# Kernel optimization log

Hardware: AMD Instinct MI355X
Metric: run time of the kernel (lower is better)

The kernel has to match this reference:

```python
import math
import jax, jax.numpy as jnp
from jax import lax
import numpy as np

B, C, M, N = 8, 512, 64, 64
DN = ('NCHW', 'OIHW', 'NCHW')


def dct_mat(n):
    # Orthonormal DCT-II basis, matching the torch construction.
    i = jnp.arange(n, dtype=jnp.float32)
    A = jnp.cos(jnp.outer(i, i + 0.5) * (math.pi / n)) * np.float32(math.sqrt(2.0 / n))
    return A.at[0].divide(np.float32(math.sqrt(2.0)))


def setup_inputs() -> dict:
    key = jax.random.key(0)
    ks = jax.random.split(key, 7)
    s = 0.05
    x = jax.random.normal(ks[0], (B, C, M, N), dtype=jnp.float32)
    # 4 conv branches, each: 1x1 512->128, 3x3 dil=2 128->128, 1x1 128->128
    W1 = jax.random.normal(ks[1], (4, 128, 512, 1, 1), dtype=jnp.float32) * s
    b1 = jax.random.normal(ks[2], (4, 128), dtype=jnp.float32) * s
    W2 = jax.random.normal(ks[3], (4, 128, 128, 3, 3), dtype=jnp.float32) * s
    b2 = jax.random.normal(ks[4], (4, 128), dtype=jnp.float32) * s
    W3 = jax.random.normal(ks[5], (4, 128, 128, 1, 1), dtype=jnp.float32) * s
    b3 = jax.random.normal(ks[6], (4, 128), dtype=jnp.float32) * s
    return {"x": x, "W1": W1, "b1": b1, "W2": W2, "b2": b2, "W3": W3, "b3": b3}


def dct3d_topk(x):
    b, c, m, n = x.shape
    Ac, Ar, Ak = dct_mat(n), dct_mat(m), dct_mat(c)
    # separable 3D DCT: along N, then M, then C
    t = jnp.einsum('kn,bcmn->bcmk', Ac, x)
    t = jnp.einsum('km,bcmn->bckn', Ar, t)
    D = jnp.einsum('kc,bcmn->bkmn', Ak, t)
    total = b * c * m * n
    absD = jnp.abs(D)
    s = jnp.sort(absD.reshape(-1))  # ascending; kth-largest = s[total-k]
    recons = []
    for k in (total // 4, total // 16, total // 64, total // 256):
        thr = s[total - k]
        Dm = jnp.where(absD >= thr, D, jnp.float32(0))
        y = jnp.einsum('kc,bkmn->bcmn', Ak, Dm)   # inverse along C
        y = jnp.einsum('km,bckn->bcmn', Ar, y)    # inverse along M
        y = jnp.einsum('kn,bcmk->bcmn', Ac, y)    # inverse along N
        recons.append(y)
    return jnp.stack(recons)  # [4, B, C, M, N]


def conv_branch(h, w1, c1, w2, c2, w3, c3):
    h = lax.conv_general_dilated(h, w1, (1, 1), 'VALID', dimension_numbers=DN)
    h = jax.nn.relu(h + c1[None, :, None, None])
    h = lax.conv_general_dilated(h, w2, (1, 1), ((2, 2), (2, 2)), rhs_dilation=(2, 2), dimension_numbers=DN)
    h = jax.nn.relu(h + c2[None, :, None, None])
    h = lax.conv_general_dilated(h, w3, (1, 1), 'VALID', dimension_numbers=DN)
    return jax.nn.relu(h + c3[None, :, None, None])


def reference(x, W1, b1, W2, b2, W3, b3):
    d = dct3d_topk(x)
    outs = [conv_branch(d[i], W1[i], b1[i], W2[i], b2[i], W3[i], b3[i]) for i in range(4)]
    w = jax.nn.softmax(jnp.concatenate(outs, axis=1), axis=1)
    return x * w + x
```

## Files before the change

### kernel.cpp

```cpp
#include <hip/hip_runtime.h>
#include <math.h>

#define NB   8
#define NC   512
#define SP   4096
#define TOT  16777216L
static const double PI_D = 3.14159265358979323846;

typedef short s16x8 __attribute__((ext_vector_type(8)));
typedef float f32x4 __attribute__((ext_vector_type(4)));
typedef unsigned short u16;

#define OFF_T    0L
#define OFF_CAND 0L
#define OFF_CNT  8388608L
#define OFF_P2   8392704L
#define OFF_P3   9441280L
#define OFF_H2R  9965568L
#define OFF_H3R  9969664L
#define OFF_GF   9971712L
#define OFF_H1P  0L
#define OFF_X2   8388608L
#define OFF_THI  16777216L
#define OFF_H1   16777216L
#define OFF_D    25165824L
#define OFF_H2   25165824L
#define OFF_AKFH 41943040L
#define OFF_AKFL 42074112L
#define OFF_AKH  42205184L
#define OFF_AKL  42336256L
#define OFF_ACT  42467328L
#define OFF_GBF  42468352L
#define OFF_W2A  42599424L
#define OFF_W3B  42894336L
#define OFF_HIST 42927104L
#define OFF_SEL  42937344L
#define OFF_THR  42937360L
#define OFF_ACH  42937368L
#define OFF_ACL  42939416L

__device__ inline u16 bfr(float x) {
    unsigned u = __float_as_uint(x);
    unsigned r = u + 0x7fffu + ((u >> 16) & 1u);
    return (u16)(r >> 16);
}
__device__ inline float bff(u16 h) { return __uint_as_float(((unsigned)h) << 16); }

#define MFMA(a, b, c) __builtin_amdgcn_mfma_f32_16x16x32_bf16((a), (b), (c), 0, 0, 0)

__global__ void k_ctab(float* __restrict__ ctab) {
    int m = blockIdx.x * 256 + threadIdx.x;
    if (m < 2048) ctab[m] = (float)cos(PI_D * (double)m / 1024.0);
}

__global__ void k_build_mats(const float* __restrict__ ctab,
                             u16* __restrict__ Akh, u16* __restrict__ Akl,
                             u16* __restrict__ Akfh, u16* __restrict__ Akfl,
                             u16* __restrict__ AcT, u16* __restrict__ Ach, u16* __restrict__ Acl) {
    int idx = blockIdx.x * 256 + threadIdx.x;
    if (idx < 512 * 512) {
        int i = idx >> 9, j = idx & 511;
        float c = ctab[(i * (2 * j + 1)) & 2047];
        float f = c * (i == 0 ? 0.04419417382415922f : 0.0625f);
        u16 h = bfr(f);
        u16 l = bfr(f - bff(h));
        Akh[idx] = h;
        Akl[idx] = l;
        long fa = ((long)(i >> 4) * 16 + (j >> 5)) * 512 + ((j >> 3) & 3) * 128 + (i & 15) * 8 + (j & 7);
        Akfh[fa] = h;
        Akfl[fa] = l;
    }
    if (idx < 64 * 64) {
        int i = idx >> 6, j = idx & 63;
        float c = ctab[(8 * i * (2 * j + 1)) & 2047];
        float a = c * (i == 0 ? 0.125f : 0.17677669529663687f);
        u16 ah = bfr(a);
        Ach[idx] = ah;
        Acl[idx] = bfr(a - bff(ah));
        int n = idx >> 6, np = idx & 63;
        float w = ctab[(8 * np * (2 * n + 1)) & 2047];
        AcT[idx] = bfr(w * (np == 0 ? 0.125f : 0.17677669529663687f));
    }
}

__global__ void k_zero(unsigned* __restrict__ p, int n) {
    int i = blockIdx.x * 256 + threadIdx.x;
    if (i < n) p[i] = 0u;
}

__global__ __launch_bounds__(256, 2) void k_gmm(const float* __restrict__ W1,
                                                const u16* __restrict__ Akh, const u16* __restrict__ Akl,
                                                u16* __restrict__ G) {
    __shared__ __align__(16) short Wh[128 * 40];
    __shared__ __align__(16) short Wl[128 * 40];
    __shared__ __align__(16) short Qh[128 * 40];
    __shared__ __align__(16) short Ql[128 * 40];
    const int p0 = blockIdx.y * 128, kc0 = blockIdx.x * 128;
    const int tid = threadIdx.x;
    const int lane = tid & 63, wave = tid >> 6;
    const int fr = lane & 15, qd = lane >> 4;
    const int mq = (wave >> 1) * 64, nq = (wave & 1) * 64;
    f32x4 acc[4][4];
#pragma unroll
    for (int i = 0; i < 4; ++i)
#pragma unroll
        for (int j = 0; j < 4; ++j) acc[i][j] = (f32x4){0.f, 0.f, 0.f, 0.f};
    const float* Pg = W1 + (long)p0 * 512;
    const u16* Qgh = Akh + (long)kc0 * 512;
    const u16* Qgl = Akl + (long)kc0 * 512;
    const int r0 = tid >> 2, q40 = (tid & 3) * 8;
    float4 pa4[2], pb4[2];
    s16x8 qsh[2], qsl[2];
#pragma unroll
    for (int j = 0; j < 2; ++j) {
        int r = r0 + j * 64;
        const float* src = &Pg[(long)r * 512 + q40];
        pa4[j] = *(const float4*)src;
        pb4[j] = *(const float4*)(src + 4);
        qsh[j] = *(const s16x8*)&Qgh[(long)r * 512 + q40];
        qsl[j] = *(const s16x8*)&Qgl[(long)r * 512 + q40];
    }
    for (int ch = 0; ch < 16; ++ch) {
        __syncthreads();
#pragma unroll
        for (int j = 0; j < 2; ++j) {
            int r = r0 + j * 64;
            float f[8] = {pa4[j].x, pa4[j].y, pa4[j].z, pa4[j].w,
                          pb4[j].x, pb4[j].y, pb4[j].z, pb4[j].w};
            s16x8 vh, vl;
#pragma unroll
            for (int q = 0; q < 8; ++q) {
                u16 h = bfr(f[q]);
                vh[q] = (short)h;
                vl[q] = (short)bfr(f[q] - bff(h));
            }
            *(s16x8*)&Wh[r * 40 + q40] = vh;
            *(s16x8*)&Wl[r * 40 + q40] = vl;
            *(s16x8*)&Qh[r * 40 + q40] = qsh[j];
            *(s16x8*)&Ql[r * 40 + q40] = qsl[j];
        }
        __syncthreads();
        if (ch < 15) {
            const int kn = (ch + 1) * 32;
#pragma unroll
            for (int j = 0; j < 2; ++j) {
                int r = r0 + j * 64;
                const float* src = &Pg[(long)r * 512 + kn + q40];
                pa4[j] = *(const float4*)src;
                pb4[j] = *(const float4*)(src + 4);
                qsh[j] = *(const s16x8*)&Qgh[(long)r * 512 + kn + q40];
                qsl[j] = *(const s16x8*)&Qgl[(long)r * 512 + kn + q40];
            }
        }
// ... 129 lines not shown
    }
#pragma unroll
    for (int i = 0; i < 2; ++i)
#pragma unroll
        for (int j = 0; j < 2; ++j) {
            int k1 = nq + 16 * j + fr;
            int mb = mq + 16 * i + qd * 4;
            ushort4 ph, pl;
            float v0 = a1[i][j][0], v1 = a1[i][j][1], v2 = a1[i][j][2], v3 = a1[i][j][3];
            ph.x = bfr(v0); ph.y = bfr(v1); ph.z = bfr(v2); ph.w = bfr(v3);
            pl.x = bfr(v0 - bff(ph.x)); pl.y = bfr(v1 - bff(ph.y));
            pl.z = bfr(v2 - bff(ph.z)); pl.w = bfr(v3 - bff(ph.w));
            *(ushort4*)&Uh[k1 * 72 + mb] = ph;
            *(ushort4*)&Ul[k1 * 72 + mb] = pl;
        }
    __syncthreads();
    f32x4 a2[2][2];
#pragma unroll
    for (int i = 0; i < 2; ++i)
#pragma unroll
        for (int j = 0; j < 2; ++j) a2[i][j] = (f32x4){0.f, 0.f, 0.f, 0.f};
#pragma unroll
    for (int ks = 0; ks < 2; ++ks) {
        const int k0 = ks * 32 + qd * 8;
        s16x8 uh[2], ul[2];
#pragma unroll
        for (int i = 0; i < 2; ++i) {
            uh[i] = *(const s16x8*)&Uh[(mq + 16 * i + fr) * 72 + k0];
            ul[i] = *(const s16x8*)&Ul[(mq + 16 * i + fr) * 72 + k0];
        }
#pragma unroll
        for (int j = 0; j < 2; ++j) {
            s16x8 qh = *(const s16x8*)&Ah[(nq + 16 * j + fr) * 72 + k0];
            s16x8 ql = *(const s16x8*)&Al[(nq + 16 * j + fr) * 72 + k0];
#pragma unroll
            for (int i = 0; i < 2; ++i) {
                a2[i][j] = MFMA(uh[i], qh, a2[i][j]);
                a2[i][j] = MFMA(uh[i], ql, a2[i][j]);
                a2[i][j] = MFMA(ul[i], qh, a2[i][j]);
            }
        }
    }
#pragma unroll
    for (int i = 0; i < 2; ++i)
#pragma unroll
        for (int j = 0; j < 2; ++j) {
            int k2 = nq + 16 * j + fr;
            int nb = mq + 16 * i + qd * 4;
            ushort4 pk;
            pk.x = bfr(a2[i][j][0]); pk.y = bfr(a2[i][j][1]);
            pk.z = bfr(a2[i][j][2]); pk.w = bfr(a2[i][j][3]);
            *(ushort4*)&dst[k2 * 64 + nb] = pk;
        }
}

__global__ __launch_bounds__(256) void k_tsplit(const u16* __restrict__ t16,
                                                u16* __restrict__ thi) {
    __shared__ float Ls[64][65];
    const int b = blockIdx.z, cg = blockIdx.y, pg = blockIdx.x;
    const int tid = threadIdx.x;
    const u16* src = t16 + ((long)b * 512 + cg * 64) * 4096 + pg * 64;
#pragma unroll
    for (int j = 0; j < 2; ++j) {
        int idx = tid + j * 256;
        int c = idx >> 3, p8 = (idx & 7) * 8;
        s16x8 v = *(const s16x8*)&src[(long)c * 4096 + p8];
#pragma unroll
        for (int q = 0; q < 8; ++q) Ls[c][p8 + q] = bff((u16)v[q]);
    }
    __syncthreads();
#pragma unroll
    for (int j = 0; j < 2; ++j) {
        int idx = tid + j * 256;
        int p = idx >> 3, c8 = idx & 7;
        s16x8 vh;
#pragma unroll
        for (int q = 0; q < 8; ++q) vh[q] = (short)bfr(Ls[c8 * 8 + q][p]);
        long addr = ((long)b * 4096 + pg * 64 + p) * 512 + cg * 64 + c8 * 8;
        *(s16x8*)&thi[addr] = vh;
    }
}

__global__ __launch_bounds__(256, 4) void k_cgemm(const u16* __restrict__ thi,
                                                  const u16* __restrict__ Akfh, const u16* __restrict__ Akfl,
                                                  float* __restrict__ D, unsigned* __restrict__ g1) {
    __shared__ __align__(16) short Ph[128 * 40];
    __shared__ unsigned hh[2048];
    const int b = blockIdx.z;
    const int p0 = blockIdx.y * 128, kc0 = blockIdx.x * 128;
    const int tid = threadIdx.x;
    const int lane = tid & 63, wave = tid >> 6;
    const int fr = lane & 15, qd = lane >> 4;
    const int mq = (wave >> 1) * 64, nq = (wave & 1) * 64;
    for (int t = tid; t < 2048; t += 256) hh[t] = 0u;
    f32x4 acc[4][4];
#pragma unroll
    for (int i = 0; i < 4; ++i)
#pragma unroll
        for (int j = 0; j < 4; ++j) acc[i][j] = (f32x4){0.f, 0.f, 0.f, 0.f};
    const u16* Pgh = thi + ((long)b * 4096 + p0) * 512;
    const int r0 = tid >> 2, q40 = (tid & 3) * 8;
    s16x8 psh[2];
#pragma unroll
    for (int j = 0; j < 2; ++j)
        psh[j] = *(const s16x8*)&Pgh[(long)(r0 + j * 64) * 512 + q40];
    const long qb0 = ((long)(kc0 >> 4) + (nq >> 4)) * 16 * 512 + (long)lane * 8;
    for (int ch = 0; ch < 16; ++ch) {
        __syncthreads();
#pragma unroll
        for (int j = 0; j < 2; ++j)
            *(s16x8*)&Ph[(r0 + j * 64) * 40 + q40] = psh[j];
        __syncthreads();
        if (ch < 15) {
            const int kn = (ch + 1) * 32;
#pragma unroll
            for (int j = 0; j < 2; ++j)
                psh[j] = *(const s16x8*)&Pgh[(long)(r0 + j * 64) * 512 + kn + q40];
        }
        const long qbase = qb0 + (long)ch * 512;
        s16x8 qfh[4], qfl[4];
#pragma unroll
        for (int j = 0; j < 4; ++j) {
            qfh[j] = *(const s16x8*)&Akfh[qbase + (long)j * 8192];
            qfl[j] = *(const s16x8*)&Akfl[qbase + (long)j * 8192];
        }
#pragma unroll
        for (int i = 0; i < 4; ++i) {
            s16x8 ph = *(const s16x8*)&Ph[(mq + 16 * i + fr) * 40 + qd * 8];
#pragma unroll
            for (int j = 0; j < 4; ++j) {
                acc[i][j] = MFMA(ph, qfh[j], acc[i][j]);
                acc[i][j] = MFMA(ph, qfl[j], acc[i][j]);
            }
        }
    }
#pragma unroll
    for (int i = 0; i < 4; ++i)
#pragma unroll
        for (int j = 0; j < 4; ++j) {
            int rowb = mq + 16 * i + qd * 4;
            int col = kc0 + nq + 16 * j + fr;
#pragma unroll
            for (int r = 0; r < 4; ++r) {
                float v = acc[i][j][r];
                D[((long)b * 4096 + p0 + rowb + r) * 512 + col] = v;
                unsigned bin = __float_as_uint(fabsf(v)) >> 19;
                atomicAdd(&hh[bin & 2047u], 1u << ((bin >> 11) << 4));
            }
        }
    __syncthreads();
    for (int t = tid; t < 2048; t += 256) {
        unsigned c = hh[t];
        unsigned lo = c & 0xffffu, hi = c >> 16;
        if (lo) atomicAdd(&g1[t], lo);
        if (hi) atomicAdd(&g1[t + 2048], hi);
    }
}

__global__ void k_scan1(const unsigned* __restrict__ hist, unsigned* __restrict__ sel) {
    __shared__ unsigned chunk[256];
    __shared__ unsigned above[256];
    const int t = threadIdx.x;
    unsigned s = 0;
#pragma unroll
    for (int j = 0; j < 16; ++j) s += hist[t * 16 + j];
    chunk[t] = s;
    __syncthreads();
    if (t == 0) {
        unsigned a = 0;
        for (int c = 255; c >= 0; --c) { above[c] = a; a += chunk[c]; }
    }
    __syncthreads();
    const unsigned kv[4] = {4194304u, 1048576u, 262144u, 65536u};
    unsigned run = above[t];
    for (int j = 15; j >= 0; --j) {
        unsigned bin = t * 16 + j;
        unsigned hb = hist[bin];
        unsigned Sab = run;
        run += hb;
#pragma unroll
        for (int i = 0; i < 4; ++i)
            if (run >= kv[i] && Sab < kv[i]) { sel[i] = bin; sel[4 + i] = kv[i] - Sab; }
    }
}

__global__ __launch_bounds__(256) void k_compact(const float4* __restrict__ D,
                                                 const unsigned* __restrict__ sel,
                                                 unsigned* __restrict__ cand,
                                                 unsigned* __restrict__ cnt) {
    __shared__ unsigned lctr;
    if (threadIdx.x == 0) lctr = 0u;
    __syncthreads();
    const unsigned p0 = sel[0], p1 = sel[1], p2 = sel[2], p3 = sel[3];
    const int lane = threadIdx.x & 63;
    unsigned* slice = cand + (long)blockIdx.x * 4096;
    const long n4 = TOT / 4;
    for (long idx = (long)blockIdx.x * 256 + threadIdx.x; idx < n4; idx += (long)gridDim.x * 256) {
        float4 v = D[idx];
        float f[4] = {v.x, v.y, v.z, v.w};
#pragma unroll
        for (int q = 0; q < 4; ++q) {
            unsigned u = __float_as_uint(fabsf(f[q]));
            unsigned pre = u >> 19;
            bool m = (pre == p0) | (pre == p1) | (pre == p2) | (pre == p3);
            unsigned long long mask = __ballot(m);
            if (mask) {
                int leader = __ffsll((long long)mask) - 1;
                unsigned base = 0;
                if (lane == leader) base = atomicAdd(&lctr, (unsigned)__popcll(mask));
                base = (unsigned)__shfl((int)base, leader);
                if (m) {
                    unsigned pos = base + (unsigned)__popcll(mask & ((1ULL << lane) - 1ULL));
                    if (pos < 4096u) slice[pos] = u;
                }
            }
        }
    }
    __syncthreads();
    if (threadIdx.x == 0) cnt[blockIdx.x] = lctr < 4096u ? lctr : 4096u;
}

__global__ __launch_bounds__(256) void k_hist2c(const unsigned* __restrict__ cand,
                                                const unsigned* __restrict__ cnt,
                                                const unsigned* __restrict__ sel,
                                                unsigned* __restrict__ partial) {
    __shared__ unsigned h[4096];
    for (int i = threadIdx.x; i < 4096; i += 256) h[i] = 0u;
    __syncthreads();
    const unsigned p0 = sel[0], p1 = sel[1], p2 = sel[2], p3 = sel[3];
    for (int s = 0; s < 8; ++s) {
        int slice = blockIdx.x * 8 + s;
        unsigned n = cnt[slice];
        const unsigned* L = cand + (long)slice * 4096;
        for (unsigned i = threadIdx.x; i < n; i += 256) {
            unsigned u = L[i];
            unsigned pre = u >> 19, mid = (u >> 9) & 1023u;
            if (pre == p0) atomicAdd(&h[mid], 1u);
            else if (pre == p1) atomicAdd(&h[1024 + mid], 1u);
            else if (pre == p2) atomicAdd(&h[2048 + mid], 1u);
            else if (pre == p3) atomicAdd(&h[3072 + mid], 1u);
        }
    }
    __syncthreads();
    unsigned* dst = partial + (long)blockIdx.x * 4096;
    for (int i = threadIdx.x; i < 4096; i += 256) dst[i] = h[i];
}

__global__ __launch_bounds__(256) void k_red(const unsigned* __restrict__ partial,
                                             unsigned* __restrict__ out, int nbins, int nrows) {
    int bin = blockIdx.x * 256 + threadIdx.x;
    if (bin >= nbins) return;
    unsigned s = 0;
#pragma unroll 16
    for (int r = 0; r < nrows; ++r) s += partial[(long)r * nbins + bin];
    out[bin] = s;
}

__global__ void k_scan2(const unsigned* __restrict__ hist2, unsigned* __restrict__ sel) {
    __shared__ unsigned chunk[256];
    __shared__ unsigned above[256];
    const int t = threadIdx.x;
    for (int i = 0; i < 4; ++i) {
        const unsigned* h = hist2 + i * 1024;
        unsigned r = sel[4 + i];
        unsigned s = h[t * 4] + h[t * 4 + 1] + h[t * 4 + 2] + h[t * 4 + 3];
        chunk[t] = s;
        __syncthreads();
        if (t == 0) {
            unsigned a = 0;
            for (int c = 255; c >= 0; --c) { above[c] = a; a += chunk[c]; }
        }
        __syncthreads();
        unsigned run = above[t];
        for (int j = 3; j >= 0; --j) {
            unsigned bin = t * 4 + j;
            unsigned hb = h[bin];
            unsigned Sab = run;
            run += hb;
            if (run >= r && Sab < r) { sel[8 + i] = bin; sel[12 + i] = r - Sab; }
        }
        __syncthreads();
    }
}

__global__ __launch_bounds__(256) void k_hist3c(const unsigned* __restrict__ cand,
                                                const unsigned* __restrict__ cnt,
                                                const unsigned* __restrict__ sel,
                                                unsigned* __restrict__ partial) {
    __shared__ unsigned h[2048];
    for (int i = threadIdx.x; i < 2048; i += 256) h[i] = 0u;
    __syncthreads();
    unsigned pre2[4];
#pragma unroll
    for (int i = 0; i < 4; ++i) pre2[i] = (sel[i] << 10) | sel[8 + i];
    for (int s = 0; s < 8; ++s) {
        int slice = blockIdx.x * 8 + s;
        unsigned n = cnt[slice];
        const unsigned* L = cand + (long)slice * 4096;
        for (unsigned i = threadIdx.x; i < n; i += 256) {
            unsigned u = L[i];
            unsigned p = u >> 9, low = u & 511u;
            if (p == pre2[0]) atomicAdd(&h[low], 1u);
            else if (p == pre2[1]) atomicAdd(&h[512 + low], 1u);
            else if (p == pre2[2]) atomicAdd(&h[1024 + low], 1u);
            else if (p == pre2[3]) atomicAdd(&h[1536 + low], 1u);
        }
    }
    __syncthreads();
    unsigned* dst = partial + (long)blockIdx.x * 2048;
    for (int i = threadIdx.x; i < 2048; i += 256) dst[i] = h[i];
}

__global__ void k_scan3(const unsigned* __restrict__ hist3, const unsigned* __restrict__ sel,
                        float* __restrict__ thr) {
    __shared__ unsigned chunk[256];
    __shared__ unsigned above[256];
    const int t = threadIdx.x;
    for (int i = 0; i < 4; ++i) {
        const unsigned* h = hist3 + i * 512;
        unsigned r = sel[12 + i];
        unsigned s = h[t * 2] + h[t * 2 + 1];
        chunk[t] = s;
        __syncthreads();
        if (t == 0) {
            unsigned a = 0;
            for (int c = 255; c >= 0; --c) { above[c] = a; a += chunk[c]; }
        }
        __syncthreads();
        unsigned run = above[t];
        for (int j = 1; j >= 0; --j) {
            unsigned bin = t * 2 + j;
            unsigned hb = h[bin];
            unsigned Sab = run;
            run += hb;
            if (run >= r && Sab < r)
                thr[i] = __uint_as_float((sel[i] << 19) | (sel[8 + i] << 9) | bin);
        }
        __syncthreads();
    }
}

__global__ __launch_bounds__(256, 4) void k_conv1(const float* __restrict__ D, const u16* __restrict__ Gf,
                                                  const float* __restrict__ thrp, u16* __restrict__ h1pre) {
    __shared__ __align__(16) short Pt[128 * 40];
    const int b = blockIdx.z, br = blockIdx.y, p0 = blockIdx.x * 128;
    const int z2 = br * 8 + b;
    const float thr = thrp[br];
    const int tid = threadIdx.x;
    const int lane = tid & 63, wave = tid >> 6;
    const int fr = lane & 15, qd = lane >> 4;
    const int mq = (wave >> 1) * 64, nq = (wave & 1) * 64;
    f32x4 acc[4][4];
#pragma unroll
    for (int i = 0; i < 4; ++i)
#pragma unroll
        for (int j = 0; j < 4; ++j) acc[i][j] = (f32x4){0.f, 0.f, 0.f, 0.f};
    const float* Pg = D + ((long)b * 4096 + p0) * 512;
    const int r0 = tid >> 2, q40 = (tid & 3) * 8;
    float4 da[2], db[2];
#pragma unroll
    for (int j = 0; j < 2; ++j) {
        const float* src = &Pg[(long)(r0 + j * 64) * 512 + q40];
        da[j] = *(const float4*)src;
        db[j] = *(const float4*)(src + 4);
    }
    const long qb0 = (((long)br * 16) * 8 + (nq >> 4)) * 512 + (long)lane * 8;
    for (int ch = 0; ch < 16; ++ch) {
        const int k0 = ch * 32;
        __syncthreads();
#pragma unroll
        for (int j = 0; j < 2; ++j) {
            int r = r0 + j * 64;
            s16x8 m;
            float f[8] = {da[j].x, da[j].y, da[j].z, da[j].w, db[j].x, db[j].y, db[j].z, db[j].w};
#pragma unroll
            for (int q = 0; q < 8; ++q) m[q] = (short)(fabsf(f[q]) >= thr ? bfr(f[q]) : (u16)0);
            *(s16x8*)&Pt[r * 40 + q40] = m;
        }
        __syncthreads();
        if (ch < 15) {
            const int kn = k0 + 32;
#pragma unroll
            for (int j = 0; j < 2; ++j) {
                const float* src = &Pg[(long)(r0 + j * 64) * 512 + kn + q40];
                da[j] = *(const float4*)src;
                db[j] = *(const float4*)(src + 4);
            }
        }
        const long qbase = qb0 + (long)ch * 4096;
        s16x8 qb[4];
#pragma unroll
        for (int j = 0; j < 4; ++j) qb[j] = *(const s16x8*)&Gf[qbase + (long)j * 512];
#pragma unroll
        for (int i = 0; i < 4; ++i) {
            s16x8 pa = *(const s16x8*)&Pt[(mq + 16 * i + fr) * 40 + qd * 8];
#pragma unroll
            for (int j = 0; j < 4; ++j) acc[i][j] = MFMA(pa, qb[j], acc[i][j]);
        }
    }
#pragma unroll
    for (int i = 0; i < 4; ++i)
#pragma unroll
        for (int j = 0; j < 4; ++j) {
            int rowb = p0 + mq + 16 * i + qd * 4;
            int o = nq + 16 * j + fr;
            ushort4 pk;
            pk.x = bfr(acc[i][j][0]); pk.y = bfr(acc[i][j][1]);
            pk.z = bfr(acc[i][j][2]); pk.w = bfr(acc[i][j][3]);
            *(ushort4*)&h1pre[((long)z2 * 128 + o) * 4096 + rowb] = pk;
        }
}

__global__ __launch_bounds__(256, 4) void k_idct1(const u16* __restrict__ h1pre, const u16* __restrict__ AcT,
                                                  u16* __restrict__ X2) {
    __shared__ __align__(16) short Pt[128 * 72];
    __shared__ __align__(16) short Qt[64 * 72];
    const int b = blockIdx.z, br = blockIdx.y, m0 = blockIdx.x * 128;
    const int z2 = br * 8 + b;
    const int tid = threadIdx.x;
    const int lane = tid & 63, wave = tid >> 6;
    const int fr = lane & 15, qd = lane >> 4;
    const int mq = wave * 32;
    const u16* Pg = h1pre + (long)z2 * 524288 + (long)m0 * 64;
    f32x4 acc[2][4];
#pragma unroll
    for (int i = 0; i < 2; ++i)
#pragma unroll
        for (int j = 0; j < 4; ++j) acc[i][j] = (f32x4){0.f, 0.f, 0.f, 0.f};
#pragma unroll
    for (int j = 0; j < 4; ++j) {
        int idx = tid + j * 256;
        int r = idx >> 3, q8 = (idx & 7) * 8;
        *(s16x8*)&Pt[r * 72 + q8] = *(const s16x8*)&Pg[(long)r * 64 + q8];
    }
#pragma unroll
    for (int j = 0; j < 2; ++j) {
        int idx = tid + j * 256;
        int r = idx >> 3, q8 = (idx & 7) * 8;
        *(s16x8*)&Qt[r * 72 + q8] = *(const s16x8*)&AcT[(long)r * 64 + q8];
    }
    __syncthreads();
#pragma unroll
    for (int ks = 0; ks < 2; ++ks) {
        s16x8 pa[2], qb[4];
#pragma unroll
        for (int i = 0; i < 2; ++i) pa[i] = *(const s16x8*)&Pt[(mq + 16 * i + fr) * 72 + ks * 32 + qd * 8];
#pragma unroll
        for (int j = 0; j < 4; ++j) qb[j] = *(const s16x8*)&Qt[(16 * j + fr) * 72 + ks * 32 + qd * 8];
#pragma unroll
        for (int i = 0; i < 2; ++i)
#pragma unroll
            for (int j = 0; j < 4; ++j) acc[i][j] = MFMA(pa[i], qb[j], acc[i][j]);
    }
#pragma unroll
    for (int i = 0; i < 2; ++i)
#pragma unroll
        for (int j = 0; j < 4; ++j) {
            int Rb = m0 + mq + 16 * i + qd * 4;
            int o = Rb >> 6, y = Rb & 63;
            int xo = 16 * j + fr;
            ushort4 pk;
            pk.x = bfr(acc[i][j][0]); pk.y = bfr(acc[i][j][1]);
            pk.z = bfr(acc[i][j][2]); pk.w = bfr(acc[i][j][3]);
            *(ushort4*)&X2[(long)z2 * 524288 + ((long)xo * 128 + o) * 64 + y] = pk;
        }
}

__global__ __launch_bounds__(256, 4) void k_idct2(const u16* __restrict__ X2, const u16* __restrict__ AcT,
                                                  const float* __restrict__ b1, u16* __restrict__ h1) {
    __shared__ __align__(16) short Pt[128 * 72];
// ... 190 lines not shown
}

__global__ __launch_bounds__(256) void k_final(const float* __restrict__ x, const u16* __restrict__ lgn,
                                               float* __restrict__ out) {
    const int b = blockIdx.y, m = blockIdx.x;
    const int tid = threadIdx.x;
    const int csub = tid >> 3, oct = tid & 7;
    const u16* L = lgn + ((long)b * 64 + m) * 512 * 64;
    __shared__ float redm[32][64];
    __shared__ float reds[32][64];
    __shared__ float Mf[64], Sf[64];
    float mx[8], sm[8];
#pragma unroll
    for (int q = 0; q < 8; ++q) { mx[q] = -1e30f; sm[q] = 0.f; }
#pragma unroll 4
    for (int k = 0; k < 16; ++k) {
        int c = csub * 16 + k;
        s16x8 v8 = *(const s16x8*)&L[c * 64 + oct * 8];
#pragma unroll
        for (int q = 0; q < 8; ++q) {
            float v = bff((u16)v8[q]);
            float mn = fmaxf(mx[q], v);
            sm[q] = sm[q] * __expf(mx[q] - mn) + __expf(v - mn);
            mx[q] = mn;
        }
    }
#pragma unroll
    for (int q = 0; q < 8; ++q) {
        redm[csub][oct * 8 + q] = mx[q];
        reds[csub][oct * 8 + q] = sm[q];
    }
    __syncthreads();
    if (tid < 64) {
        float M = -1e30f;
#pragma unroll 8
        for (int g = 0; g < 32; ++g) M = fmaxf(M, redm[g][tid]);
        float S = 0.f;
#pragma unroll 8
        for (int g = 0; g < 32; ++g) S += reds[g][tid] * __expf(redm[g][tid] - M);
        Mf[tid] = M;
        Sf[tid] = 1.0f / S;
    }
    __syncthreads();
    float Mv[8], Iv[8];
#pragma unroll
    for (int q = 0; q < 8; ++q) { Mv[q] = Mf[oct * 8 + q]; Iv[q] = Sf[oct * 8 + q]; }
    const long xb = (long)b * 512 * 4096 + m * 64 + oct * 8;
#pragma unroll 4
    for (int k = 0; k < 16; ++k) {
        int c = csub * 16 + k;
        s16x8 v8 = *(const s16x8*)&L[c * 64 + oct * 8];
        long a = xb + (long)c * 4096;
        float4 x0 = *(const float4*)&x[a];
        float4 x1 = *(const float4*)&x[a + 4];
        float xf[8] = {x0.x, x0.y, x0.z, x0.w, x1.x, x1.y, x1.z, x1.w};
        float r[8];
#pragma unroll
        for (int q = 0; q < 8; ++q) {
            float w = __expf(bff((u16)v8[q]) - Mv[q]) * Iv[q];
            r[q] = xf[q] * w + xf[q];
        }
        *(float4*)&out[a] = make_float4(r[0], r[1], r[2], r[3]);
        *(float4*)&out[a + 4] = make_float4(r[4], r[5], r[6], r[7]);
    }
}

extern "C" void kernel_launch(void* const* d_in, const int* in_sizes, int n_in,
                              void* d_out, int out_size, void* d_ws, size_t ws_size,
                              hipStream_t stream) {
    (void)in_sizes; (void)n_in; (void)out_size; (void)ws_size;
    const float* x  = (const float*)d_in[0];
    const float* W1 = (const float*)d_in[1];
    const float* b1 = (const float*)d_in[2];
    const float* W2 = (const float*)d_in[3];
    const float* b2 = (const float*)d_in[4];
    const float* W3 = (const float*)d_in[5];
    const float* b3 = (const float*)d_in[6];
    float* out = (float*)d_out;
    float* ws = (float*)d_ws;

    u16*   t16  = (u16*)(ws + OFF_T);
    unsigned* cand = (unsigned*)(ws + OFF_CAND);
    unsigned* cnt  = (unsigned*)(ws + OFF_CNT);
    unsigned* p2   = (unsigned*)(ws + OFF_P2);
    unsigned* p3   = (unsigned*)(ws + OFF_P3);
    unsigned* h2r  = (unsigned*)(ws + OFF_H2R);
    unsigned* h3r  = (unsigned*)(ws + OFF_H3R);
    u16*   h1pre= (u16*)(ws + OFF_H1P);
    u16*   lgn  = (u16*)(ws + OFF_H1P);
    u16*   X2   = (u16*)(ws + OFF_X2);
    u16*   thi  = (u16*)(ws + OFF_THI);
    u16*   h1   = (u16*)(ws + OFF_H1);
    u16*   Akfh = (u16*)(ws + OFF_AKFH);
    u16*   Akfl = (u16*)(ws + OFF_AKFL);
    u16*   Gf   = (u16*)(ws + OFF_GF);
    float* D    = ws + OFF_D;
    float* ctab = ws + OFF_D;
    u16*   h2   = (u16*)(ws + OFF_H2);
    u16*   Akh  = (u16*)(ws + OFF_AKH);
    u16*   Akl  = (u16*)(ws + OFF_AKL);
    u16*   AcT  = (u16*)(ws + OFF_ACT);
    u16*   Gb   = (u16*)(ws + OFF_GBF);
    u16*   W2f  = (u16*)(ws + OFF_W2A);
    u16*   W3f  = (u16*)(ws + OFF_W3B);
    unsigned* hist1 = (unsigned*)(ws + OFF_HIST);
    unsigned* sel   = (unsigned*)(ws + OFF_SEL);
    float* thr      = ws + OFF_THR;
    u16*   Ach  = (u16*)(ws + OFF_ACH);
    u16*   Acl  = (u16*)(ws + OFF_ACL);

    k_ctab<<<8, 256, 0, stream>>>(ctab);
    k_build_mats<<<1024, 256, 0, stream>>>(ctab, Akh, Akl, Akfh, Akfl, AcT, Ach, Acl);
    k_zero<<<16, 256, 0, stream>>>(hist1, 4096);
    k_gmm<<<dim3(4, 4), 256, 0, stream>>>(W1, Akh, Akl, Gb);
    k_gf<<<128, 256, 0, stream>>>(Gb, Gf);
    k_wprep<<<2304, 256, 0, stream>>>(W2, W3, W2f, W3f);

    k_tile_fwd<<<4096, 256, 0, stream>>>(x, t16, Ach, Acl);
    k_tsplit<<<dim3(64, 8, 8), 256, 0, stream>>>(t16, thi);
    k_cgemm<<<dim3(4, 32, 8), 256, 0, stream>>>(thi, Akfh, Akfl, D, hist1);

    k_scan1<<<1, 256, 0, stream>>>(hist1, sel);
    k_compact<<<2048, 256, 0, stream>>>((const float4*)D, sel, cand, cnt);
    k_hist2c<<<256, 256, 0, stream>>>(cand, cnt, sel, p2);
    k_red<<<16, 256, 0, stream>>>(p2, h2r, 4096, 256);
    k_scan2<<<1, 256, 0, stream>>>(h2r, sel);
    k_hist3c<<<256, 256, 0, stream>>>(cand, cnt, sel, p3);
    k_red<<<8, 256, 0, stream>>>(p3, h3r, 2048, 256);
    k_scan3<<<1, 256, 0, stream>>>(h3r, sel, thr);

    k_conv1<<<dim3(32, 4, 8), 256, 0, stream>>>(D, Gf, thr, h1pre);
    k_idct1<<<dim3(64, 4, 8), 256, 0, stream>>>(h1pre, AcT, X2);
    k_idct2<<<dim3(64, 4, 8), 256, 0, stream>>>(X2, AcT, b1, h1);
    k_conv2<<<dim3(32, 4, 8), 256, 0, stream>>>(h1, W2f, b2, h2);
    k_conv3<<<dim3(32, 4, 8), 256, 0, stream>>>(h2, W3f, b3, lgn);

    k_final<<<dim3(64, 8), 256, 0, stream>>>(x, lgn, out);
}
```

Baseline: 485.6 us.

## Store DCT coefficients as bf16 and simplify top-k threshold selection

The C-axis DCT GEMM now writes its output D as bf16 instead of fp32, halving that buffer's write traffic and the reads in the compact and conv1 stages. Because each bf16 value has only 16 bits, the three-level radix select collapses to a coarse histogram plus an 8-bin suffix histogram, which removes several histogram, reduce and scan kernels. The GEMM also stages the Ak hi/lo operands through shared memory from the row-major matrices instead of reading a pre-swizzled fragment layout. The risk is that thresholding on rounded bf16 magnitudes changes which coefficients pass the top-k cut when values tie at that precision.

```diff
diff --git a/kernel.cpp b/kernel.cpp
--- a/kernel.cpp
+++ b/kernel.cpp
@@ -14,10 +14,6 @@
 #define OFF_T    0L
 #define OFF_CAND 0L
 #define OFF_CNT  8388608L
-#define OFF_P2   8392704L
-#define OFF_P3   9441280L
-#define OFF_H2R  9965568L
-#define OFF_H3R  9969664L
 #define OFF_GF   9971712L
 #define OFF_H1P  0L
 #define OFF_X2   8388608L
@@ -25,8 +21,6 @@
 #define OFF_H1   16777216L
 #define OFF_D    25165824L
 #define OFF_H2   25165824L
-#define OFF_AKFH 41943040L
-#define OFF_AKFL 42074112L
 #define OFF_AKH  42205184L
 #define OFF_AKL  42336256L
 #define OFF_ACT  42467328L
@@ -35,7 +29,6 @@
 #define OFF_W3B  42894336L
 #define OFF_HIST 42927104L
 #define OFF_SEL  42937344L
-#define OFF_THR  42937360L
 #define OFF_ACH  42937368L
 #define OFF_ACL  42939416L
 
@@ -55,7 +48,6 @@
 
 __global__ void k_build_mats(const float* __restrict__ ctab,
                              u16* __restrict__ Akh, u16* __restrict__ Akl,
-                             u16* __restrict__ Akfh, u16* __restrict__ Akfl,
                              u16* __restrict__ AcT, u16* __restrict__ Ach, u16* __restrict__ Acl) {
     int idx = blockIdx.x * 256 + threadIdx.x;
     if (idx < 512 * 512) {
@@ -63,12 +55,8 @@
         float c = ctab[(i * (2 * j + 1)) & 2047];
         float f = c * (i == 0 ? 0.04419417382415922f : 0.0625f);
         u16 h = bfr(f);
-        u16 l = bfr(f - bff(h));
         Akh[idx] = h;
-        Akl[idx] = l;
-        long fa = ((long)(i >> 4) * 16 + (j >> 5)) * 512 + ((j >> 3) & 3) * 128 + (i & 15) * 8 + (j & 7);
-        Akfh[fa] = h;
-        Akfl[fa] = l;
+        Akl[idx] = bfr(f - bff(h));
     }
     if (idx < 64 * 64) {
         int i = idx >> 6, j = idx & 63;
@@ -364,9 +352,11 @@
 }
 
 __global__ __launch_bounds__(256, 4) void k_cgemm(const u16* __restrict__ thi,
-                                                  const u16* __restrict__ Akfh, const u16* __restrict__ Akfl,
-                                                  float* __restrict__ D, unsigned* __restrict__ g1) {
+                                                  const u16* __restrict__ Akh, const u16* __restrict__ Akl,
+                                                  u16* __restrict__ D16, unsigned* __restrict__ g1) {
     __shared__ __align__(16) short Ph[128 * 40];
+    __shared__ __align__(16) short Qh[128 * 40];
+    __shared__ __align__(16) short Ql[128 * 40];
     __shared__ unsigned hh[2048];
     const int b = blockIdx.z;
     const int p0 = blockIdx.y * 128, kc0 = blockIdx.x * 128;
@@ -381,30 +371,42 @@
 #pragma unroll
         for (int j = 0; j < 4; ++j) acc[i][j] = (f32x4){0.f, 0.f, 0.f, 0.f};
     const u16* Pgh = thi + ((long)b * 4096 + p0) * 512;
+    const u16* Qgh = Akh + (long)kc0 * 512;
+    const u16* Qgl = Akl + (long)kc0 * 512;
     const int r0 = tid >> 2, q40 = (tid & 3) * 8;
-    s16x8 psh[2];
-#pragma unroll
-    for (int j = 0; j < 2; ++j)
-        psh[j] = *(const s16x8*)&Pgh[(long)(r0 + j * 64) * 512 + q40];
-    const long qb0 = ((long)(kc0 >> 4) + (nq >> 4)) * 16 * 512 + (long)lane * 8;
+    s16x8 psh[2], qsh[2], qsl[2];
+#pragma unroll
+    for (int j = 0; j < 2; ++j) {
+        int r = r0 + j * 64;
+        psh[j] = *(const s16x8*)&Pgh[(long)r * 512 + q40];
+        qsh[j] = *(const s16x8*)&Qgh[(long)r * 512 + q40];
+        qsl[j] = *(const s16x8*)&Qgl[(long)r * 512 + q40];
+    }
     for (int ch = 0; ch < 16; ++ch) {
         __syncthreads();
 #pragma unroll
-        for (int j = 0; j < 2; ++j)
-            *(s16x8*)&Ph[(r0 + j * 64) * 40 + q40] = psh[j];
+        for (int j = 0; j < 2; ++j) {
+            int r = r0 + j * 64;
+            *(s16x8*)&Ph[r * 40 + q40] = psh[j];
+            *(s16x8*)&Qh[r * 40 + q40] = qsh[j];
+            *(s16x8*)&Ql[r * 40 + q40] = qsl[j];
+        }
         __syncthreads();
         if (ch < 15) {
             const int kn = (ch + 1) * 32;
 #pragma unroll
-            for (int j = 0; j < 2; ++j)
-                psh[j] = *(const s16x8*)&Pgh[(long)(r0 + j * 64) * 512 + kn + q40];
-        }
-        const long qbase = qb0 + (long)ch * 512;
+            for (int j = 0; j < 2; ++j) {
+                int r = r0 + j * 64;
+                psh[j] = *(const s16x8*)&Pgh[(long)r * 512 + kn + q40];
+                qsh[j] = *(const s16x8*)&Qgh[(long)r * 512 + kn + q40];
+                qsl[j] = *(const s16x8*)&Qgl[(long)r * 512 + kn + q40];
+            }
+        }
         s16x8 qfh[4], qfl[4];
 #pragma unroll
         for (int j = 0; j < 4; ++j) {
-            qfh[j] = *(const s16x8*)&Akfh[qbase + (long)j * 8192];
-            qfl[j] = *(const s16x8*)&Akfl[qbase + (long)j * 8192];
+            qfh[j] = *(const s16x8*)&Qh[(nq + 16 * j + fr) * 40 + qd * 8];
+            qfl[j] = *(const s16x8*)&Ql[(nq + 16 * j + fr) * 40 + qd * 8];
         }
 #pragma unroll
         for (int i = 0; i < 4; ++i) {
@@ -424,9 +426,9 @@
             int col = kc0 + nq + 16 * j + fr;
 #pragma unroll
             for (int r = 0; r < 4; ++r) {
-                float v = acc[i][j][r];
-                D[((long)b * 4096 + p0 + rowb + r) * 512 + col] = v;
-                unsigned bin = __float_as_uint(fabsf(v)) >> 19;
+                u16 pk = bfr(acc[i][j][r]);
+                D16[((long)b * 4096 + p0 + rowb + r) * 512 + col] = pk;
+                unsigned bin = (((unsigned)pk) & 0x7fffu) >> 3;
                 atomicAdd(&hh[bin & 2047u], 1u << ((bin >> 11) << 4));
             }
         }
@@ -466,7 +468,7 @@
     }
 }
 
-__global__ __launch_bounds__(256) void k_compact(const float4* __restrict__ D,
+__global__ __launch_bounds__(256) void k_compact(const u16* __restrict__ D16,
                                                  const unsigned* __restrict__ sel,
                                                  unsigned* __restrict__ cand,
                                                  unsigned* __restrict__ cnt) {
@@ -476,14 +478,13 @@
     const unsigned p0 = sel[0], p1 = sel[1], p2 = sel[2], p3 = sel[3];
     const int lane = threadIdx.x & 63;
     unsigned* slice = cand + (long)blockIdx.x * 4096;
-    const long n4 = TOT / 4;
-    for (long idx = (long)blockIdx.x * 256 + threadIdx.x; idx < n4; idx += (long)gridDim.x * 256) {
-        float4 v = D[idx];
-        float f[4] = {v.x, v.y, v.z, v.w};
-#pragma unroll
-        for (int q = 0; q < 4; ++q) {
-            unsigned u = __float_as_uint(fabsf(f[q]));
-            unsigned pre = u >> 19;
+    const long n8 = TOT / 8;
+    for (long idx = (long)blockIdx.x * 256 + threadIdx.x; idx < n8; idx += (long)gridDim.x * 256) {
+        s16x8 v = *(const s16x8*)&D16[idx * 8];
+#pragma unroll
+        for (int q = 0; q < 8; ++q) {
+            unsigned u = (unsigned)(unsigned short)v[q];
+            unsigned pre = (u & 0x7fffu) >> 3;
             bool m = (pre == p0) | (pre == p1) | (pre == p2) | (pre == p3);
             unsigned long long mask = __ballot(m);
             if (mask) {
@@ -502,12 +503,12 @@
     if (threadIdx.x == 0) cnt[blockIdx.x] = lctr < 4096u ? lctr : 4096u;
 }
 
-__global__ __launch_bounds__(256) void k_hist2c(const unsigned* __restrict__ cand,
-                                                const unsigned* __restrict__ cnt,
-                                                const unsigned* __restrict__ sel,
-                                                unsigned* __restrict__ partial) {
-    __shared__ unsigned h[4096];
-    for (int i = threadIdx.x; i < 4096; i += 256) h[i] = 0u;
+__global__ __launch_bounds__(256) void k_histsuf(const unsigned* __restrict__ cand,
+                                                 const unsigned* __restrict__ cnt,
+                                                 const unsigned* __restrict__ sel,
+                                                 unsigned* __restrict__ h2) {
+    __shared__ unsigned h[32];
+    if (threadIdx.x < 32) h[threadIdx.x] = 0u;
     __syncthreads();
     const unsigned p0 = sel[0], p1 = sel[1], p2 = sel[2], p3 = sel[3];
     for (int s = 0; s < 8; ++s) {
@@ -515,119 +516,41 @@
         unsigned n = cnt[slice];
         const unsigned* L = cand + (long)slice * 4096;
         for (unsigned i = threadIdx.x; i < n; i += 256) {
-            unsigned u = L[i];
-            unsigned pre = u >> 19, mid = (u >> 9) & 1023u;
-            if (pre == p0) atomicAdd(&h[mid], 1u);
-            else if (pre == p1) atomicAdd(&h[1024 + mid], 1u);
-            else if (pre == p2) atomicAdd(&h[2048 + mid], 1u);
-            else if (pre == p3) atomicAdd(&h[3072 + mid], 1u);
-        }
-    }
-    __syncthreads();
-    unsigned* dst = partial + (long)blockIdx.x * 4096;
-    for (int i = threadIdx.x; i < 4096; i += 256) dst[i] = h[i];
-}
-
-__global__ __launch_bounds__(256) void k_red(const unsigned* __restrict__ partial,
-                                             unsigned* __restrict__ out, int nbins, int nrows) {
-    int bin = blockIdx.x * 256 + threadIdx.x;
-    if (bin >= nbins) return;
-    unsigned s = 0;
-#pragma unroll 16
-    for (int r = 0; r < nrows; ++r) s += partial[(long)r * nbins + bin];
-    out[bin] = s;
-}
-
-__global__ void k_scan2(const unsigned* __restrict__ hist2, unsigned* __restrict__ sel) {
-    __shared__ unsigned chunk[256];
-    __shared__ unsigned above[256];
-    const int t = threadIdx.x;
-    for (int i = 0; i < 4; ++i) {
-        const unsigned* h = hist2 + i * 1024;
-        unsigned r = sel[4 + i];
-        unsigned s = h[t * 4] + h[t * 4 + 1] + h[t * 4 + 2] + h[t * 4 + 3];
-        chunk[t] = s;
-        __syncthreads();
-        if (t == 0) {
-            unsigned a = 0;
-            for (int c = 255; c >= 0; --c) { above[c] = a; a += chunk[c]; }
-        }
-        __syncthreads();
-        unsigned run = above[t];
-        for (int j = 3; j >= 0; --j) {
-            unsigned bin = t * 4 + j;
-            unsigned hb = h[bin];
-            unsigned Sab = run;
-            run += hb;
-            if (run >= r && Sab < r) { sel[8 + i] = bin; sel[12 + i] = r - Sab; }
-        }
-        __syncthreads();
-    }
-}
-
-__global__ __launch_bounds__(256) void k_hist3c(const unsigned* __restrict__ cand,
-                                                const unsigned* __restrict__ cnt,
-                                                const unsigned* __restrict__ sel,
-                                                unsigned* __restrict__ partial) {
-    __shared__ unsigned h[2048];
-    for (int i = threadIdx.x; i < 2048; i += 256) h[i] = 0u;
-    __syncthreads();
-    unsigned pre2[4];
-#pragma unroll
-    for (int i = 0; i < 4; ++i) pre2[i] = (sel[i] << 10) | sel[8 + i];
-    for (int s = 0; s < 8; ++s) {
-        int slice = blockIdx.x * 8 + s;
-        unsigned n = cnt[slice];
-        const unsigned* L = cand + (long)slice * 4096;
-        for (unsigned i = threadIdx.x; i < n; i += 256) {
-            unsigned u = L[i];
-            unsigned p = u >> 9, low = u & 511u;
-            if (p == pre2[0]) atomicAdd(&h[low], 1u);
-            else if (p == pre2[1]) atomicAdd(&h[512 + low], 1u);
-            else if (p == pre2[2]) atomicAdd(&h[1024 + low], 1u);
-            else if (p == pre2[3]) atomicAdd(&h[1536 + low], 1u);
-        }
-    }
-    __syncthreads();
-    unsigned* dst = partial + (long)blockIdx.x * 2048;
-    for (int i = threadIdx.x; i < 2048; i += 256) dst[i] = h[i];
-}
-
-__global__ void k_scan3(const unsigned* __restrict__ hist3, const unsigned* __restrict__ sel,
-                        float* __restrict__ thr) {
-    __shared__ unsigned chunk[256];
-    __shared__ unsigned above[256];
-    const int t = threadIdx.x;
-    for (int i = 0; i < 4; ++i) {
-        const unsigned* h = hist3 + i * 512;
-        unsigned r = sel[12 + i];
-        unsigned s = h[t * 2] + h[t * 2 + 1];
-        chunk[t] = s;
-        __syncthreads();
-        if (t == 0) {
-            unsigned a = 0;
-            for (int c = 255; c >= 0; --c) { above[c] = a; a += chunk[c]; }
-        }
-        __syncthreads();
-        unsigned run = above[t];
-        for (int j = 1; j >= 0; --j) {
-            unsigned bin = t * 2 + j;
-            unsigned hb = h[bin];
-            unsigned Sab = run;
-            run += hb;
-            if (run >= r && Sab < r)
-                thr[i] = __uint_as_float((sel[i] << 19) | (sel[8 + i] << 9) | bin);
-        }
-        __syncthreads();
-    }
-}
-
-__global__ __launch_bounds__(256, 4) void k_conv1(const float* __restrict__ D, const u16* __restrict__ Gf,
-                                                  const float* __restrict__ thrp, u16* __restrict__ h1pre) {
+            unsigned u = L[i] & 0x7fffu;
+            unsigned pre = u >> 3, suf = u & 7u;
+            if (pre == p0) atomicAdd(&h[suf], 1u);
+            else if (pre == p1) atomicAdd(&h[8 + suf], 1u);
+            else if (pre == p2) atomicAdd(&h[16 + suf], 1u);
+            else if (pre == p3) atomicAdd(&h[24 + suf], 1u);
+        }
+    }
+    __syncthreads();
+    if (threadIdx.x < 32) {
+        unsigned c = h[threadIdx.x];
+        if (c) atomicAdd(&h2[threadIdx.x], c);
+    }
+}
+
+__global__ void k_scansuf(const unsigned* __restrict__ h2, unsigned* __restrict__ sel) {
+    int t = threadIdx.x;
+    if (t < 4) {
+        unsigned r = sel[4 + t];
+        unsigned run = 0, thr = 0;
+        for (int s = 7; s >= 0; --s) {
+            unsigned c = h2[t * 8 + s];
+            if (run < r && run + c >= r) thr = (sel[t] << 3) | (unsigned)s;
+            run += c;
+        }
+        sel[8 + t] = thr;
+    }
+}
+
+__global__ __launch_bounds__(256, 4) void k_conv1(const u16* __restrict__ D16, const u16* __restrict__ Gf,
+                                                  const unsigned* __restrict__ sel, u16* __restrict__ h1pre) {
     __shared__ __align__(16) short Pt[128 * 40];
     const int b = blockIdx.z, br = blockIdx.y, p0 = blockIdx.x * 128;
     const int z2 = br * 8 + b;
-    const float thr = thrp[br];
+    const unsigned thrp = sel[8 + br];
     const int tid = threadIdx.x;
     const int lane = tid & 63, wave = tid >> 6;
     const int fr = lane & 15, qd = lane >> 4;
@@ -637,15 +560,12 @@
     for (int i = 0; i < 4; ++i)
 #pragma unroll
         for (int j = 0; j < 4; ++j) acc[i][j] = (f32x4){0.f, 0.f, 0.f, 0.f};
-    const float* Pg = D + ((long)b * 4096 + p0) * 512;
+    const u16* Pg = D16 + ((long)b * 4096 + p0) * 512;
     const int r0 = tid >> 2, q40 = (tid & 3) * 8;
-    float4 da[2], db[2];
-#pragma unroll
-    for (int j = 0; j < 2; ++j) {
-        const float* src = &Pg[(long)(r0 + j * 64) * 512 + q40];
-        da[j] = *(const float4*)src;
-        db[j] = *(const float4*)(src + 4);
-    }
+    s16x8 dv[2];
+#pragma unroll
+    for (int j = 0; j < 2; ++j)
+        dv[j] = *(const s16x8*)&Pg[(long)(r0 + j * 64) * 512 + q40];
     const long qb0 = (((long)br * 16) * 8 + (nq >> 4)) * 512 + (long)lane * 8;
     for (int ch = 0; ch < 16; ++ch) {
         const int k0 = ch * 32;
@@ -654,20 +574,19 @@
         for (int j = 0; j < 2; ++j) {
             int r = r0 + j * 64;
             s16x8 m;
-            float f[8] = {da[j].x, da[j].y, da[j].z, da[j].w, db[j].x, db[j].y, db[j].z, db[j].w};
-#pragma unroll
-            for (int q = 0; q < 8; ++q) m[q] = (short)(fabsf(f[q]) >= thr ? bfr(f[q]) : (u16)0);
+#pragma unroll
+            for (int q = 0; q < 8; ++q) {
+                unsigned mag = ((unsigned)(unsigned short)dv[j][q]) & 0x7fffu;
+                m[q] = (mag >= thrp) ? dv[j][q] : (short)0;
+            }
             *(s16x8*)&Pt[r * 40 + q40] = m;
         }
         __syncthreads();
         if (ch < 15) {
             const int kn = k0 + 32;
 #pragma unroll
-            for (int j = 0; j < 2; ++j) {
-                const float* src = &Pg[(long)(r0 + j * 64) * 512 + kn + q40];
-                da[j] = *(const float4*)src;
-                db[j] = *(const float4*)(src + 4);
-            }
+            for (int j = 0; j < 2; ++j)
+                dv[j] = *(const s16x8*)&Pg[(long)(r0 + j * 64) * 512 + kn + q40];
         }
         const long qbase = qb0 + (long)ch * 4096;
         s16x8 qb[4];
@@ -1024,19 +943,13 @@
     u16*   t16  = (u16*)(ws + OFF_T);
     unsigned* cand = (unsigned*)(ws + OFF_CAND);
     unsigned* cnt  = (unsigned*)(ws + OFF_CNT);
-    unsigned* p2   = (unsigned*)(ws + OFF_P2);
-    unsigned* p3   = (unsigned*)(ws + OFF_P3);
-    unsigned* h2r  = (unsigned*)(ws + OFF_H2R);
-    unsigned* h3r  = (unsigned*)(ws + OFF_H3R);
     u16*   h1pre= (u16*)(ws + OFF_H1P);
     u16*   lgn  = (u16*)(ws + OFF_H1P);
     u16*   X2   = (u16*)(ws + OFF_X2);
     u16*   thi  = (u16*)(ws + OFF_THI);
     u16*   h1   = (u16*)(ws + OFF_H1);
-    u16*   Akfh = (u16*)(ws + OFF_AKFH);
-    u16*   Akfl = (u16*)(ws + OFF_AKFL);
     u16*   Gf   = (u16*)(ws + OFF_GF);
-    float* D    = ws + OFF_D;
+    u16*   D16  = (u16*)(ws + OFF_D);
     float* ctab = ws + OFF_D;
     u16*   h2   = (u16*)(ws + OFF_H2);
     u16*   Akh  = (u16*)(ws + OFF_AKH);
@@ -1046,32 +959,28 @@
     u16*   W2f  = (u16*)(ws + OFF_W2A);
     u16*   W3f  = (u16*)(ws + OFF_W3B);
     unsigned* hist1 = (unsigned*)(ws + OFF_HIST);
+    unsigned* h2r2  = (unsigned*)(ws + OFF_HIST) + 4096;
     unsigned* sel   = (unsigned*)(ws + OFF_SEL);
-    float* thr      = ws + OFF_THR;
     u16*   Ach  = (u16*)(ws + OFF_ACH);
     u16*   Acl  = (u16*)(ws + OFF_ACL);
 
     k_ctab<<<8, 256, 0, stream>>>(ctab);
-    k_build_mats<<<1024, 256, 0, stream>>>(ctab, Akh, Akl, Akfh, Akfl, AcT, Ach, Acl);
-    k_zero<<<16, 256, 0, stream>>>(hist1, 4096);
+    k_build_mats<<<1024, 256, 0, stream>>>(ctab, Akh, Akl, AcT, Ach, Acl);
+    k_zero<<<17, 256, 0, stream>>>(hist1, 4128);
     k_gmm<<<dim3(4, 4), 256, 0, stream>>>(W1, Akh, Akl, Gb);
     k_gf<<<128, 256, 0, stream>>>(Gb, Gf);
     k_wprep<<<2304, 256, 0, stream>>>(W2, W3, W2f, W3f);
 
     k_tile_fwd<<<4096, 256, 0, stream>>>(x, t16, Ach, Acl);
     k_tsplit<<<dim3(64, 8, 8), 256, 0, stream>>>(t16, thi);
-    k_cgemm<<<dim3(4, 32, 8), 256, 0, stream>>>(thi, Akfh, Akfl, D, hist1);
+    k_cgemm<<<dim3(4, 32, 8), 256, 0, stream>>>(thi, Akh, Akl, D16, hist1);
 
     k_scan1<<<1, 256, 0, stream>>>(hist1, sel);
-    k_compact<<<2048, 256, 0, stream>>>((const float4*)D, sel, cand, cnt);
-    k_hist2c<<<256, 256, 0, stream>>>(cand, cnt, sel, p2);
-    k_red<<<16, 256, 0, stream>>>(p2, h2r, 4096, 256);
-    k_scan2<<<1, 256, 0, stream>>>(h2r, sel);
-    k_hist3c<<<256, 256, 0, stream>>>(cand, cnt, sel, p3);
-    k_red<<<8, 256, 0, stream>>>(p3, h3r, 2048, 256);
-    k_scan3<<<1, 256, 0, stream>>>(h3r, sel, thr);
-
-    k_conv1<<<dim3(32, 4, 8), 256, 0, stream>>>(D, Gf, thr, h1pre);
+    k_compact<<<2048, 256, 0, stream>>>(D16, sel, cand, cnt);
+    k_histsuf<<<256, 256, 0, stream>>>(cand, cnt, sel, h2r2);
+    k_scansuf<<<1, 64, 0, stream>>>(h2r2, sel);
+
+    k_conv1<<<dim3(32, 4, 8), 256, 0, stream>>>(D16, Gf, sel, h1pre);
     k_idct1<<<dim3(64, 4, 8), 256, 0, stream>>>(h1pre, AcT, X2);
     k_idct2<<<dim3(64, 4, 8), 256, 0, stream>>>(X2, AcT, b1, h1);
     k_conv2<<<dim3(32, 4, 8), 256, 0, stream>>>(h1, W2f, b2, h2);
```

Result: faster. 419.4 us (-13.6%).
